# Kernel tuning notes

Measured on AMD Instinct MI355X. Metric: run time of the kernel, lower is better.

The kernel has to match this reference:

```python
import jax, jax.numpy as jnp
import numpy as np

N, D = 8192, 1024
TEMPERATURE = 0.1
EPS = 1e-8

def setup_inputs() -> dict:
    key = jax.random.key(0)
    k1, k2 = jax.random.split(key)
    emb = jax.random.normal(k1, (N, D), dtype=jnp.float32)
    # docstring: embeddings are normalized
    emb = emb / jnp.linalg.norm(emb, axis=1, keepdims=True)
    labels = jax.random.randint(k2, (N,), 0, 2, dtype=jnp.int32)
    return {"embeddings": emb, "labels": labels}

def reference(embeddings, labels):
    lab = labels.astype(embeddings.dtype)            # (N,)
    sim = jnp.matmul(embeddings, embeddings.T) / TEMPERATURE  # (N, N)
    exp_sim = jnp.exp(sim)                           # original uses raw exp (no max-subtract)
    diag = jnp.diagonal(exp_sim)                     # self-similarity exp(1/T)
    # all_sim excludes self; pos_sim = other reference rows (labels==1, j != i)
    all_sum = exp_sim.sum(axis=1) - diag             # (N,)
    pos_sum = exp_sim @ lab - diag * lab             # subtract self only when i is ref
    loss_per_row = -jnp.log(pos_sum / (all_sum + EPS))
    n_ref = lab.sum()
    loss = jnp.sum(jnp.where(lab > 0, loss_per_row, 0.0)) / jnp.maximum(n_ref, 1.0)
    # original returns 0.0 when fewer than 2 reference rows
    return jnp.where(n_ref < 2, jnp.array(0.0, embeddings.dtype), loss)
```

## Files before the change

### kernel.cpp

```cpp
#include <hip/hip_runtime.h>
#include <hip/hip_bf16.h>
#include <cstdint>
#include <cstddef>

#define NROWS 8192
#define DIM   1024
#define BT    256
#define BK    64
#define NKT   (DIM / BK)
#define NFULL 496
#define NDD   16
#define NBLK  (NFULL + NDD)
#define EPS 1e-8f
#define PRESCALE 3.798288f

#define ABUF_E 16384
#define BUF_E  32768

typedef short  bf16x8  __attribute__((ext_vector_type(8)));
typedef float  floatx4 __attribute__((ext_vector_type(4)));

typedef __attribute__((address_space(1))) const void CGV;
typedef __attribute__((address_space(3))) void LV;

__device__ __forceinline__ void async_load16(const void* g, void* l) {
    __builtin_amdgcn_global_load_lds((CGV*)g, (LV*)l, 16, 0, 0);
}

__device__ __forceinline__ unsigned short f2bf_rne(float f) {
    union { float f; unsigned u; } c; c.f = f;
    unsigned u = c.u;
    unsigned r = (u + 0x7fffu + ((u >> 16) & 1u)) >> 16;
    return (unsigned short)r;
}

__global__ __launch_bounds__(256) void convert_kernel(
    const float* __restrict__ in, unsigned short* __restrict__ out,
    float* __restrict__ accum )
{
    int i = (blockIdx.x * 256 + threadIdx.x) * 4;
    float4 v = *(const float4*)(in + i);
    ushort4 o;
    o.x = f2bf_rne(v.x * PRESCALE);
    o.y = f2bf_rne(v.y * PRESCALE);
    o.z = f2bf_rne(v.z * PRESCALE);
    o.w = f2bf_rne(v.w * PRESCALE);
    *(ushort4*)(out + i) = o;
    if (blockIdx.x < (2 * NROWS) / 256)
        accum[blockIdx.x * 256 + threadIdx.x] = 0.0f;
}

template<bool DIAG>
__device__ __forceinline__ void run_tile(
    const unsigned short* __restrict__ E,
    const int*            __restrict__ labels,
    float*                __restrict__ all_sum,
    float*                __restrict__ pos_sum,
    unsigned short* S, int rBase, int cBase)
{
    const int tid  = threadIdx.x;
    const int lane = tid & 63;
    const int w    = tid >> 6;
    const int wm   = w >> 2;
    const int wn   = (w < 4) ? w : ((0x1023 >> ((w & 3) * 4)) & 0xF);
    const int colw = lane & 15;
    const int quad = lane >> 4;
    const int swz  = colw & 7;
    const int cs0  = ((0 | quad) ^ swz) << 3;
    const int cs1  = ((4 | quad) ^ swz) << 3;

    const int l8  = lane >> 3;
    const int gch = (lane & 7) ^ l8;
    const unsigned short* gA = E + (size_t)(rBase + w * 8 + l8) * DIM + gch * 8;
    const unsigned short* gB = E + (size_t)(cBase + w * 8 + l8) * DIM + gch * 8;
    const int ldsT = w * 512 + lane * 8;

#define STG_A(rb, T, dB) async_load16(gA + (size_t)(rb) * DIM + (T) * BK,   \
                                      &S[(dB) + (rb) * 64 + ldsT])
#define STG_B(rb, T, dB) async_load16(gB + (size_t)(rb) * DIM + (T) * BK,   \
                                      &S[(dB) + ABUF_E + (rb) * 64 + ldsT])

    unsigned liveMask = 0xFFFFFFFFu;
    if (DIAG) {
        liveMask = 0u;
        #pragma unroll
        for (int mt = 0; mt < 8; ++mt)
            #pragma unroll
            for (int nt = 0; nt < 4; ++nt)
                if (wm * 128 + mt * 16 + 15 >= wn * 64 + nt * 16)
                    liveMask |= 1u << (mt * 4 + nt);
    }

    floatx4 acc[8][4];
    #pragma unroll
    for (int i = 0; i < 8; ++i)
        #pragma unroll
        for (int j = 0; j < 4; ++j)
            acc[i][j] = (floatx4)0.0f;

    STG_A(0, 0, 0);  STG_A(128, 0, 0);
    STG_A(64, 0, 0); STG_A(192, 0, 0);
    if (!DIAG) { STG_B(0, 0, 0); STG_B(64, 0, 0);
                 STG_B(128, 0, 0); STG_B(192, 0, 0); }
    STG_A(0, 1, BUF_E); STG_A(128, 1, BUF_E);
    asm volatile("s_waitcnt vmcnt(2)" ::: "memory");
    __builtin_amdgcn_s_barrier();
    __builtin_amdgcn_sched_barrier(0);

    bf16x8 bFr[2][4];

#define PH_READB(KS, CS)                                                      \
    _Pragma("unroll")                                                         \
    for (int nt = 0; nt < 4; ++nt)                                            \
        bFr[KS][nt] = *(const bf16x8*)&S[bRegion +                            \
                          (wn * 64 + nt * 16 + colw) * BK + (CS)];

#define PH_COMPUTE(M, KS, CS)                                                 \
    {                                                                         \
        bf16x8 aF[4];                                                         \
        _Pragma("unroll")                                                     \
        for (int i = 0; i < 4; ++i)                                           \
            aF[i] = *(const bf16x8*)&S[bb +                                   \
                        (wm * 128 + ((M) * 4 + i) * 16 + colw) * BK + (CS)];  \
        __builtin_amdgcn_s_setprio(1);                                        \
        _Pragma("unroll")                                                     \
        for (int i = 0; i < 4; ++i) {                                         \
            _Pragma("unroll")                                                 \
            for (int nt = 0; nt < 4; ++nt) {                                  \
                if (!DIAG || ((liveMask >> ((((M) * 4 + i) * 4) + nt)) & 1u)) \
                    acc[(M) * 4 + i][nt] =                                    \
                        __builtin_amdgcn_mfma_f32_16x16x32_bf16(              \
                            aF[i], bFr[KS][nt], acc[(M) * 4 + i][nt], 0, 0, 0);\
            }                                                                 \
        }                                                                     \
        __builtin_amdgcn_s_setprio(0);                                        \
    }

#define BARSEQ  __builtin_amdgcn_sched_barrier(0);                            \
                __builtin_amdgcn_s_barrier();                                 \
                __builtin_amdgcn_sched_barrier(0);

    for (int kt = 0; kt < NKT; ++kt) {
        const int bb = (kt & 1) ? BUF_E : 0;
        const int nb = bb ^ BUF_E;
        const int bRegion = DIAG ? bb : (bb + ABUF_E);
        const bool s1 = (kt <= NKT - 2);
        const bool s2 = (kt <= NKT - 3);

        if (s1) {
            STG_A(64, kt + 1, nb); STG_A(192, kt + 1, nb);
            if (!DIAG) { STG_B(0, kt + 1, nb); STG_B(64, kt + 1, nb); }
        }
        PH_READB(0, cs0)
        PH_COMPUTE(0, 0, cs0)
        BARSEQ

        if (s1 && !DIAG) { STG_B(128, kt + 1, nb); STG_B(192, kt + 1, nb); }
        PH_READB(1, cs1)
        PH_COMPUTE(0, 1, cs1)
        BARSEQ

        if (s2) { STG_A(0, kt + 2, bb); STG_A(128, kt + 2, bb); }
        PH_COMPUTE(1, 0, cs0)
        BARSEQ

        PH_COMPUTE(1, 1, cs1)
        __builtin_amdgcn_sched_barrier(0);
        if (s2) asm volatile("s_waitcnt vmcnt(2)" ::: "memory");
        else    asm volatile("s_waitcnt vmcnt(0)" ::: "memory");
        __builtin_amdgcn_s_barrier();
        __builtin_amdgcn_sched_barrier(0);
    }
#undef PH_COMPUTE
#undef PH_READB
#undef BARSEQ
#undef STG_A
#undef STG_B

    float labc[4];
    int   gcolv[4];
    #pragma unroll
    for (int nt = 0; nt < 4; ++nt) {
        gcolv[nt] = cBase + wn * 64 + nt * 16 + colw;
        labc[nt]  = (float)labels[gcolv[nt]];
    }

    float colAll[4] = {0.f, 0.f, 0.f, 0.f};
    float colPos[4] = {0.f, 0.f, 0.f, 0.f};

    #pragma unroll
    for (int mt = 0; mt < 8; ++mt) {
        const int growBase = rBase + wm * 128 + mt * 16 + quad * 4;
        #pragma unroll
        for (int r = 0; r < 4; ++r) {
            const int grow = growBase + r;
            const float labr = (float)labels[grow];
            float sAll = 0.f, sPos = 0.f;
            #pragma unroll
            for (int nt = 0; nt < 4; ++nt) {
                float ev = exp2f(acc[mt][nt][r]);
                ev = (grow > gcolv[nt]) ? ev : 0.0f;
                sAll += ev;
                sPos += ev * labc[nt];
                colAll[nt] += ev;
                colPos[nt] += ev * labr;
            }
            #pragma unroll
            for (int off = 1; off < 16; off <<= 1) {
                sAll += __shfl_xor(sAll, off);
                sPos += __shfl_xor(sPos, off);
            }
            if (colw == 0 && sAll != 0.f) {
                atomicAdd(&all_sum[grow], sAll);
                atomicAdd(&pos_sum[grow], sPos);
            }
        }
    }

    #pragma unroll
    for (int nt = 0; nt < 4; ++nt) {
        float aa = colAll[nt], p = colPos[nt];
        aa += __shfl_xor(aa, 16);  p += __shfl_xor(p, 16);
        aa += __shfl_xor(aa, 32);  p += __shfl_xor(p, 32);
        if (quad == 0 && aa != 0.f) {
            atomicAdd(&all_sum[gcolv[nt]], aa);
            atomicAdd(&pos_sum[gcolv[nt]], p);
        }
    }
}

__global__ __launch_bounds__(512, 2) void gemm_fused_kernel(
    const unsigned short* __restrict__ E,
    const int*            __restrict__ labels,
    float*                __restrict__ all_sum,
    float*                __restrict__ pos_sum)
{
    __shared__ __align__(16) unsigned short S[2 * BUF_E];

    const int b = blockIdx.x;
    if (b < NFULL) {
        const int t = (b & 7) * 62 + (b >> 3);
        int a = (int)((1.0f + sqrtf(1.0f + 8.0f * (float)t)) * 0.5f);
        while (a * (a - 1) / 2 > t) --a;
        while ((a + 1) * a / 2 <= t) ++a;
        const int c = t - a * (a - 1) / 2;
        run_tile<false>(E, labels, all_sum, pos_sum, S, a * BT, c * BT);
    } else {
        const int i = b - NFULL;
        for (int r = 0; r < 2; ++r) {
            const int d = (2 * i + r) * BT;
            run_tile<true>(E, labels, all_sum, pos_sum, S, d, d);
        }
    }
}

__global__ __launch_bounds__(1024) void finalize_kernel(
    const float* __restrict__ all_sum,
    const float* __restrict__ pos_sum,
    const int*   __restrict__ labels,
    float*       __restrict__ out)
{
    __shared__ float sSum[1024];
    __shared__ float sCnt[1024];
    const int tid = threadIdx.x;
    float lsum = 0.f, lcnt = 0.f;
    for (int i = tid; i < NROWS; i += 1024) {
        if (labels[i] > 0) {
            float p = pos_sum[i];
            float a = all_sum[i] + EPS;
            lsum += -logf(p / a);
            lcnt += 1.0f;
        }
    }
    sSum[tid] = lsum;
    sCnt[tid] = lcnt;
    __syncthreads();
    for (int s = 512; s > 0; s >>= 1) {
        if (tid < s) { sSum[tid] += sSum[tid + s]; sCnt[tid] += sCnt[tid + s]; }
        __syncthreads();
    }
    if (tid == 0) {
        float n = sCnt[0];
        out[0] = (n < 2.0f) ? 0.0f : sSum[0] / fmaxf(n, 1.0f);
    }
}

extern "C" void kernel_launch(void* const* d_in, const int* in_sizes, int n_in,
                              void* d_out, int out_size, void* d_ws, size_t ws_size,
                              hipStream_t stream) {
    const float* emb    = (const float*)d_in[0];
    const int*   labels = (const int*)d_in[1];
    float*       out    = (float*)d_out;

    unsigned short* Ebf = (unsigned short*)d_ws;
    const size_t embBytes = (size_t)NROWS * DIM * sizeof(unsigned short);
    float* all_sum = (float*)((char*)d_ws + embBytes);
    float* pos_sum = all_sum + NROWS;

    convert_kernel<<<(NROWS * DIM) / (4 * 256), 256, 0, stream>>>(emb, Ebf, all_sum);

    gemm_fused_kernel<<<NBLK, 512, 0, stream>>>(Ebf, labels, all_sum, pos_sum);

    finalize_kernel<<<1, 1024, 0, stream>>>(all_sum, pos_sum, labels, out);
}
```

Measured before the change: 226.6 us.

## Replace double-buffered async pipeline with single-buffer sync loop, schedule diagonal blocks first

Removes the hand-tuned double-buffered LDS pipeline (prefetching the next k-tiles during compute, with staged barriers and setprio) and replaces it with a plain single-buffer loop: sync, load the tile, sync, compute. LDS use drops by half. Diagonal blocks, which each do two tiles, now get the lowest block indices so they start first. The simpler loop gives up the overlap of global loads with MFMA work, so the kernel is likely to stall on memory each k-step.

```diff
diff --git a/kernel.cpp b/kernel.cpp
--- a/kernel.cpp
+++ b/kernel.cpp
@@ -15,7 +15,6 @@
 #define PRESCALE 3.798288f
 
 #define ABUF_E 16384
-#define BUF_E  32768
 
 typedef short  bf16x8  __attribute__((ext_vector_type(8)));
 typedef float  floatx4 __attribute__((ext_vector_type(4)));
@@ -75,11 +74,6 @@
     const unsigned short* gB = E + (size_t)(cBase + w * 8 + l8) * DIM + gch * 8;
     const int ldsT = w * 512 + lane * 8;
 
-#define STG_A(rb, T, dB) async_load16(gA + (size_t)(rb) * DIM + (T) * BK,   \
-                                      &S[(dB) + (rb) * 64 + ldsT])
-#define STG_B(rb, T, dB) async_load16(gB + (size_t)(rb) * DIM + (T) * BK,   \
-                                      &S[(dB) + ABUF_E + (rb) * 64 + ldsT])
-
     unsigned liveMask = 0xFFFFFFFFu;
     if (DIAG) {
         liveMask = 0u;
@@ -98,84 +92,47 @@
         for (int j = 0; j < 4; ++j)
             acc[i][j] = (floatx4)0.0f;
 
-    STG_A(0, 0, 0);  STG_A(128, 0, 0);
-    STG_A(64, 0, 0); STG_A(192, 0, 0);
-    if (!DIAG) { STG_B(0, 0, 0); STG_B(64, 0, 0);
-                 STG_B(128, 0, 0); STG_B(192, 0, 0); }
-    STG_A(0, 1, BUF_E); STG_A(128, 1, BUF_E);
-    asm volatile("s_waitcnt vmcnt(2)" ::: "memory");
-    __builtin_amdgcn_s_barrier();
-    __builtin_amdgcn_sched_barrier(0);
-
-    bf16x8 bFr[2][4];
-
-#define PH_READB(KS, CS)                                                      \
-    _Pragma("unroll")                                                         \
-    for (int nt = 0; nt < 4; ++nt)                                            \
-        bFr[KS][nt] = *(const bf16x8*)&S[bRegion +                            \
-                          (wn * 64 + nt * 16 + colw) * BK + (CS)];
-
-#define PH_COMPUTE(M, KS, CS)                                                 \
-    {                                                                         \
-        bf16x8 aF[4];                                                         \
-        _Pragma("unroll")                                                     \
-        for (int i = 0; i < 4; ++i)                                           \
-            aF[i] = *(const bf16x8*)&S[bb +                                   \
-                        (wm * 128 + ((M) * 4 + i) * 16 + colw) * BK + (CS)];  \
-        __builtin_amdgcn_s_setprio(1);                                        \
-        _Pragma("unroll")                                                     \
-        for (int i = 0; i < 4; ++i) {                                         \
-            _Pragma("unroll")                                                 \
-            for (int nt = 0; nt < 4; ++nt) {                                  \
-                if (!DIAG || ((liveMask >> ((((M) * 4 + i) * 4) + nt)) & 1u)) \
-                    acc[(M) * 4 + i][nt] =                                    \
-                        __builtin_amdgcn_mfma_f32_16x16x32_bf16(              \
-                            aF[i], bFr[KS][nt], acc[(M) * 4 + i][nt], 0, 0, 0);\
-            }                                                                 \
-        }                                                                     \
-        __builtin_amdgcn_s_setprio(0);                                        \
-    }
-
-#define BARSEQ  __builtin_amdgcn_sched_barrier(0);                            \
-                __builtin_amdgcn_s_barrier();                                 \
-                __builtin_amdgcn_sched_barrier(0);
+    const int bOff = DIAG ? 0 : ABUF_E;
 
     for (int kt = 0; kt < NKT; ++kt) {
-        const int bb = (kt & 1) ? BUF_E : 0;
-        const int nb = bb ^ BUF_E;
-        const int bRegion = DIAG ? bb : (bb + ABUF_E);
-        const bool s1 = (kt <= NKT - 2);
-        const bool s2 = (kt <= NKT - 3);
-
-        if (s1) {
-            STG_A(64, kt + 1, nb); STG_A(192, kt + 1, nb);
-            if (!DIAG) { STG_B(0, kt + 1, nb); STG_B(64, kt + 1, nb); }
-        }
-        PH_READB(0, cs0)
-        PH_COMPUTE(0, 0, cs0)
-        BARSEQ
-
-        if (s1 && !DIAG) { STG_B(128, kt + 1, nb); STG_B(192, kt + 1, nb); }
-        PH_READB(1, cs1)
-        PH_COMPUTE(0, 1, cs1)
-        BARSEQ
-
-        if (s2) { STG_A(0, kt + 2, bb); STG_A(128, kt + 2, bb); }
-        PH_COMPUTE(1, 0, cs0)
-        BARSEQ
-
-        PH_COMPUTE(1, 1, cs1)
-        __builtin_amdgcn_sched_barrier(0);
-        if (s2) asm volatile("s_waitcnt vmcnt(2)" ::: "memory");
-        else    asm volatile("s_waitcnt vmcnt(0)" ::: "memory");
-        __builtin_amdgcn_s_barrier();
-        __builtin_amdgcn_sched_barrier(0);
-    }
-#undef PH_COMPUTE
-#undef PH_READB
-#undef BARSEQ
-#undef STG_A
-#undef STG_B
+        __syncthreads();
+
+        const size_t gk = (size_t)kt * BK;
+        #pragma unroll
+        for (int rb = 0; rb < 256; rb += 64)
+            async_load16(gA + (size_t)rb * DIM + gk, &S[rb * 64 + ldsT]);
+        if (!DIAG) {
+            #pragma unroll
+            for (int rb = 0; rb < 256; rb += 64)
+                async_load16(gB + (size_t)rb * DIM + gk,
+                             &S[ABUF_E + rb * 64 + ldsT]);
+        }
+
+        __syncthreads();
+
+        #pragma unroll
+        for (int ksub = 0; ksub < 2; ++ksub) {
+            const int cs = ksub ? cs1 : cs0;
+            bf16x8 bF[4], aF[8];
+            #pragma unroll
+            for (int nt = 0; nt < 4; ++nt)
+                bF[nt] = *(const bf16x8*)&S[bOff +
+                              (wn * 64 + nt * 16 + colw) * BK + cs];
+            #pragma unroll
+            for (int mt = 0; mt < 8; ++mt)
+                aF[mt] = *(const bf16x8*)&S[
+                              (wm * 128 + mt * 16 + colw) * BK + cs];
+            #pragma unroll
+            for (int mt = 0; mt < 8; ++mt) {
+                #pragma unroll
+                for (int nt = 0; nt < 4; ++nt) {
+                    if (!DIAG || ((liveMask >> (mt * 4 + nt)) & 1u))
+                        acc[mt][nt] = __builtin_amdgcn_mfma_f32_16x16x32_bf16(
+                            aF[mt], bF[nt], acc[mt][nt], 0, 0, 0);
+                }
+            }
+        }
+    }
 
     float labc[4];
     int   gcolv[4];
@@ -235,22 +192,22 @@
     float*                __restrict__ all_sum,
     float*                __restrict__ pos_sum)
 {
-    __shared__ __align__(16) unsigned short S[2 * BUF_E];
+    __shared__ __align__(16) unsigned short S[2 * ABUF_E];
 
     const int b = blockIdx.x;
-    if (b < NFULL) {
-        const int t = (b & 7) * 62 + (b >> 3);
+    if (b < NDD) {
+        const int d0 = (2 * b) * BT;
+        run_tile<true>(E, labels, all_sum, pos_sum, S, d0, d0);
+        const int d1 = (2 * b + 1) * BT;
+        run_tile<true>(E, labels, all_sum, pos_sum, S, d1, d1);
+    } else {
+        const int bp = b - NDD;
+        const int t = (bp & 7) * 62 + (bp >> 3);
         int a = (int)((1.0f + sqrtf(1.0f + 8.0f * (float)t)) * 0.5f);
         while (a * (a - 1) / 2 > t) --a;
         while ((a + 1) * a / 2 <= t) ++a;
         const int c = t - a * (a - 1) / 2;
         run_tile<false>(E, labels, all_sum, pos_sum, S, a * BT, c * BT);
-    } else {
-        const int i = b - NFULL;
-        for (int r = 0; r < 2; ++r) {
-            const int d = (2 * i + r) * BT;
-            run_tile<true>(E, labels, all_sum, pos_sum, S, d, d);
-        }
     }
 }
 
```

Result: no change. 228.8 us (+1.0%).
